# Kernel optimization log

Measured on AMD Instinct MI355X. Metric: run time of the kernel, lower is better.

## Reference

```python
import jax, jax.numpy as jnp
import numpy as np

HID_DIM = 1024
B, S = 8, 2048
SCALE = float(np.sqrt(HID_DIM))
NEG = -1e10


def setup_inputs() -> dict:
    key = jax.random.key(0)
    ks = jax.random.split(key, 13)
    d = HID_DIM
    std = 1.0 / np.sqrt(d)
    return {
        "query": jax.random.normal(ks[0], (B, S, d), jnp.float32),
        "key_": jax.random.normal(ks[1], (B, S, d), jnp.float32),
        "value": jax.random.normal(ks[2], (B, S, d), jnp.float32),
        "mask": jax.random.randint(ks[3], (B, S), 0, 2, jnp.int32),
        "Wq": jax.random.uniform(ks[4], (d, d), jnp.float32, -std, std),
        "bq": jax.random.uniform(ks[5], (d,), jnp.float32, -std, std),
        "Wk": jax.random.uniform(ks[6], (d, d), jnp.float32, -std, std),
        "bk": jax.random.uniform(ks[7], (d,), jnp.float32, -std, std),
        "Wv": jax.random.uniform(ks[8], (d, d), jnp.float32, -std, std),
        "bv": jax.random.uniform(ks[9], (d,), jnp.float32, -std, std),
        "Wfc": jax.random.uniform(ks[10], (d, d), jnp.float32, -std, std),
        "bfc": jax.random.uniform(ks[11], (d,), jnp.float32, -std, std),
    }


def reference(query, key_, value, mask, Wq, bq, Wk, bk, Wv, bv, Wfc, bfc):
    # Linear projections (torch Linear: x @ W.T + b)
    Q = jnp.einsum("bsd,ed->bse", query, Wq) + bq
    K = jnp.einsum("bsd,ed->bse", key_, Wk) + bk
    V = jnp.einsum("bsd,ed->bse", value, Wv) + bv
    # Scaled dot-product energy: [B, S, S]
    energy = jnp.einsum("bqd,bkd->bqk", Q, K) / SCALE
    # Faithful to source: mask broadcast over last dim masks QUERY rows
    energy = jnp.where(mask[:, :, None] == 0, NEG, energy)
    attention = jax.nn.softmax(energy, axis=-1)  # dropout=0 (eval)
    x = jnp.einsum("bqk,bkd->bqd", attention, V)
    out = jnp.einsum("bsd,ed->bse", x, Wfc) + bfc
    return out
```

## Files before the change

kernel.cpp:

```cpp
#include <hip/hip_runtime.h>
#include <hip/hip_bf16.h>


#define DEVINL __device__ __forceinline__

typedef __bf16 bf16x8 __attribute__((ext_vector_type(8)));
typedef float f32x4 __attribute__((ext_vector_type(4)));

static constexpr int Bb = 8;
static constexpr int S = 2048;
static constexpr int D = 1024;

DEVINL unsigned short f32_to_bf16(float f) {
  unsigned u = __float_as_uint(f);
  u = (u + 0x7FFFu + ((u >> 16) & 1u)) >> 16;
  return (unsigned short)u;
}
DEVINL float bflo(unsigned u) { return __uint_as_float(u << 16); }
DEVINL float bfhi(unsigned u) { return __uint_as_float(u & 0xFFFF0000u); }

DEVINL void gload16(const unsigned short* g, char* l) {
  __builtin_amdgcn_global_load_lds((__attribute__((address_space(1))) void*)g,
                                   (__attribute__((address_space(3))) void*)l,
                                   16, 0, 0);
}
DEVINL void gload16u(const unsigned short* g, unsigned short* l) {
  gload16(g, (char*)l);
}

#define BAR() __builtin_amdgcn_s_barrier()
#define LGK0() asm volatile("s_waitcnt lgkmcnt(0)" ::: "memory")

#define PH_OPEN() \
  BAR();          \
  LGK0();         \
  __builtin_amdgcn_s_setprio(1)
#define PH_CLOSE()               \
  __builtin_amdgcn_s_setprio(0); \
  BAR()

#define MFMA_QUAD(A_, B_, MO, NO)                                              \
  {                                                                            \
    _Pragma("unroll") for (int mi_ = 0; mi_ < 4; mi_++) {                      \
      _Pragma("unroll") for (int nj_ = 0; nj_ < 2; nj_++) {                    \
        acc[(MO) + mi_][(NO) + nj_] = __builtin_amdgcn_mfma_f32_16x16x32_bf16( \
            A_[mi_][0], B_[nj_][0], acc[(MO) + mi_][(NO) + nj_], 0, 0, 0);     \
        acc[(MO) + mi_][(NO) + nj_] = __builtin_amdgcn_mfma_f32_16x16x32_bf16( \
            A_[mi_][1], B_[nj_][1], acc[(MO) + mi_][(NO) + nj_], 0, 0, 0);     \
      }                                                                        \
    }                                                                          \
  }

__global__ __launch_bounds__(256) void conv_f32_bf16(const float* __restrict__ in,
                                                     unsigned short* __restrict__ out,
                                                     int n8) {
  int i = blockIdx.x * 256 + threadIdx.x;
  int stride = gridDim.x * 256;
  for (; i < n8; i += stride) {
    const float4* p = (const float4*)in + (size_t)i * 2;
    float4 a = p[0], b = p[1];
    uint4 o;
    o.x = (unsigned)f32_to_bf16(a.x) | ((unsigned)f32_to_bf16(a.y) << 16);
    o.y = (unsigned)f32_to_bf16(a.z) | ((unsigned)f32_to_bf16(a.w) << 16);
    o.z = (unsigned)f32_to_bf16(b.x) | ((unsigned)f32_to_bf16(b.y) << 16);
    o.w = (unsigned)f32_to_bf16(b.z) | ((unsigned)f32_to_bf16(b.w) << 16);
    ((uint4*)out)[i] = o;
  }
}

__global__ __launch_bounds__(256) void tconv(const float* __restrict__ in,
                                             unsigned short* __restrict__ out,
                                             int R, int C) {
  __shared__ unsigned short t[64][72];
  const int c0 = blockIdx.x * 64, r0 = blockIdx.y * 64, b = blockIdx.z;
  in += (size_t)b * R * C;
  out += (size_t)b * R * C;
  const int tr = threadIdx.x >> 4;
  const int tc = threadIdx.x & 15;
#pragma unroll
  for (int i = 0; i < 4; i++) {
    int row = tr + i * 16;
    float4 v = *(const float4*)(in + (size_t)(r0 + row) * C + c0 + tc * 4);
    t[tc * 4 + 0][row] = f32_to_bf16(v.x);
    t[tc * 4 + 1][row] = f32_to_bf16(v.y);
    t[tc * 4 + 2][row] = f32_to_bf16(v.z);
    t[tc * 4 + 3][row] = f32_to_bf16(v.w);
  }
  __syncthreads();
  const int c = threadIdx.x >> 2, rs = (threadIdx.x & 3) * 16;
  unsigned short tmp[16];
#pragma unroll
  for (int j = 0; j < 16; j++) tmp[j] = t[c][rs + j];
  *(uint4*)(out + (size_t)(c0 + c) * R + r0 + rs) = *(const uint4*)&tmp[0];
  *(uint4*)(out + (size_t)(c0 + c) * R + r0 + rs + 8) = *(const uint4*)&tmp[8];
}

__global__ __launch_bounds__(256) void cvec_kernel(const float* __restrict__ Wfc,
                                                   const float* __restrict__ bv,
                                                   const float* __restrict__ bfc,
                                                   float* __restrict__ cv) {
  const int f = blockIdx.x;
  const float* row = Wfc + (size_t)f * 1024;
  float s = 0.f;
  for (int e = threadIdx.x; e < 1024; e += 256) s += row[e] * bv[e];
#pragma unroll
  for (int off = 32; off >= 1; off >>= 1) s += __shfl_xor(s, off);
  __shared__ float red[4];
  const int wave = threadIdx.x >> 6, lane = threadIdx.x & 63;
  if (lane == 0) red[wave] = s;
  __syncthreads();
  if (threadIdx.x == 0) cv[f] = red[0] + red[1] + red[2] + red[3] + bfc[f];
}

__global__ __launch_bounds__(256) void gvec_kernel(const unsigned short* __restrict__ WkT,
                                                   const float* __restrict__ bq,
                                                   float* __restrict__ g32) {
  const int e = blockIdx.x;
  const unsigned short* row = WkT + (size_t)e * 1024;
  const int j0 = threadIdx.x * 4;
  uint2 v = *(const uint2*)(row + j0);
  float4 b4 = *(const float4*)(bq + j0);
  float s = bflo(v.x) * b4.x + bfhi(v.x) * b4.y + bflo(v.y) * b4.z + bfhi(v.y) * b4.w;
#pragma unroll
  for (int off = 32; off >= 1; off >>= 1) s += __shfl_xor(s, off);
  __shared__ float red[4];
  const int wave = threadIdx.x >> 6, lane = threadIdx.x & 63;
  if (lane == 0) red[wave] = s;
  __syncthreads();
  if (threadIdx.x == 0) g32[e] = (red[0] + red[1] + red[2] + red[3]) * (1.0f / 32.0f);
}

__global__ __launch_bounds__(256) void wvec_kernel(const unsigned short* __restrict__ xk,
                                                   const float* __restrict__ g32,
                                                   float* __restrict__ w32) {
  const int row = blockIdx.x * 4 + (threadIdx.x >> 6);
  const int lane = threadIdx.x & 63;
  const unsigned short* r = xk + (size_t)row * 1024;
  float s = 0.f;
#pragma unroll
  for (int c = 0; c < 2; c++) {
    const int e0 = c * 512 + lane * 8;
    uint4 v = *(const uint4*)(r + e0);
    unsigned u[4] = {v.x, v.y, v.z, v.w};
#pragma unroll
    for (int i = 0; i < 4; i++) {
      float2 gg = *(const float2*)(g32 + e0 + i * 2);
      s += bflo(u[i]) * gg.x + bfhi(u[i]) * gg.y;
    }
  }
#pragma unroll
  for (int off = 32; off >= 1; off >>= 1) s += __shfl_xor(s, off);
  if (lane == 0) w32[row] = s;
}

__global__ __launch_bounds__(256) void rowinv_kernel(const float* __restrict__ partialT,
                                                     float* __restrict__ rowinv) {
  const int r = blockIdx.x * 256 + threadIdx.x;
  float s = 0.f;
#pragma unroll
  for (int c = 0; c < 16; c++) s += partialT[(size_t)c * 16384 + r];
  rowinv[r] = 1.0f / s;
}

__global__ __launch_bounds__(256) void gemm128(const unsigned short* __restrict__ A,
                                               const unsigned short* __restrict__ Bt,
                                               unsigned short* __restrict__ C,
                                               int M, int N, int K,
                                               long long bsA, long long bsB, long long bsC) {
  const int tid = threadIdx.x;
  const int wave = tid >> 6;
  const int lane = tid & 63;
  const int wr = wave >> 1, wc = wave & 1;
  const int m0 = blockIdx.y * 128, n0 = blockIdx.x * 128;
  A += (size_t)blockIdx.z * bsA;
  Bt += (size_t)blockIdx.z * bsB;
  C += (size_t)blockIdx.z * bsC;

  __shared__ unsigned short lds[2][2][128 * 32];

  const int srow = wave * 16 + (lane >> 2);
  const int scol = (lane & 3) * 8;
  const unsigned short* gA = A + (size_t)(m0 + srow) * K + scol;
  const unsigned short* gB = Bt + (size_t)(n0 + srow) * K + scol;

  f32x4 acc[4][4];
#pragma unroll
  for (int i = 0; i < 4; i++)
#pragma unroll
    for (int j = 0; j < 4; j++) acc[i][j] = (f32x4){0.f, 0.f, 0.f, 0.f};

  const int nk = K >> 5;
  auto stage = [&](int buf, int kt) {
    const unsigned short* a0 = gA + (size_t)kt * 32;
    const unsigned short* b0 = gB + (size_t)kt * 32;
    unsigned short* la = &lds[buf][0][wave * 512];
    unsigned short* lb = &lds[buf][1][wave * 512];
    gload16u(a0, la);
    gload16u(a0 + (size_t)64 * K, la + 2048);
    gload16u(b0, lb);
    gload16u(b0 + (size_t)64 * K, lb + 2048);
  };

  stage(0, 0);
  asm volatile("s_waitcnt vmcnt(0)" ::: "memory");
  __syncthreads();

  const int fm = lane & 15;
  const int fk = (lane >> 4) * 8;

  int cur = 0;
  for (int t = 0; t < nk; ++t) {
    if (t + 1 < nk) stage(cur ^ 1, t + 1);
    bf16x8 af[4], bfr[4];
#pragma unroll
    for (int i = 0; i < 4; i++)
      af[i] = *(const bf16x8*)&lds[cur][0][(wr * 64 + i * 16 + fm) * 32 + fk];
#pragma unroll
    for (int j = 0; j < 4; j++)
      bfr[j] = *(const bf16x8*)&lds[cur][1][(wc * 64 + j * 16 + fm) * 32 + fk];
#pragma unroll
    for (int i = 0; i < 4; i++)
#pragma unroll
      for (int j = 0; j < 4; j++)
        acc[i][j] = __builtin_amdgcn_mfma_f32_16x16x32_bf16(af[i], bfr[j], acc[i][j], 0, 0, 0);
    asm volatile("s_waitcnt vmcnt(0)" ::: "memory");
    __syncthreads();
    cur ^= 1;
  }

  const int en = n0 + wc * 64 + fm;
  const int em = m0 + wr * 64 + ((lane >> 4) << 2);
#pragma unroll
  for (int j = 0; j < 4; j++)
#pragma unroll
    for (int i = 0; i < 4; i++)
#pragma unroll
      for (int r = 0; r < 4; r++)
        C[(size_t)(em + i * 16 + r) * N + en + j * 16] = f32_to_bf16(acc[i][j][r]);
}

template <int OUTMODE, bool HAS_BIAS>
__global__ __launch_bounds__(512, 2) void gemm256(
    const unsigned short* __restrict__ A, const unsigned short* __restrict__ Bt,
    const float* __restrict__ bias, const int* __restrict__ msk,
    float* __restrict__ partial, void* __restrict__ Cv,
    int M, int N, int K, int lda, int ldb,
    long long bsA, long long bsB, long long bsC, float scale) {
  extern __shared__ char smem[];
  const int tid = threadIdx.x;
  const int wave = tid >> 6, lane = tid & 63;
  const int wr = wave >> 2, wc = wave & 3;

  const int gx = gridDim.x, gy = gridDim.y;
  const int nwg = gx * gy * (int)gridDim.z;
  const int wg = blockIdx.x + gx * (blockIdx.y + gy * blockIdx.z);
  const int swz = (wg & 7) * (nwg >> 3) + (wg >> 3);
  const int bx = swz % gx;
  const int rem = swz / gx;
  const int by = rem % gy;
  const int bz = rem / gy;

  const int m0 = by * 256, n0 = bx * 256;
  A += (size_t)bz * bsA;
  Bt += (size_t)bz * bsB;

  const int rl = lane >> 3;
  const int gl = (lane & 7) ^ rl;
  const unsigned short* gA = A + (size_t)(m0 + wave * 8 + rl) * lda + gl * 8;
  const unsigned short* gB = Bt + (size_t)(n0 + wave * 8 + rl) * ldb + gl * 8;

  auto stageA = [&](int db, int t, int h) {
    const unsigned short* g = gA + (size_t)(h * 128) * lda + (size_t)t * 64;
    char* l = smem + db * 65536 + h * 16384 + wave * 1024;
    gload16(g, l);
    gload16(g + (size_t)64 * lda, l + 8192);
  };
  auto stageB = [&](int db, int t, int h) {
    const unsigned short* g = gB + (size_t)(h * 128) * ldb + (size_t)t * 64;
    char* l = smem + db * 65536 + 32768 + h * 16384 + wave * 1024;
    gload16(g, l);
    gload16(g + (size_t)64 * ldb, l + 8192);
  };

  const int fr = lane & 15;
  const int fg = lane >> 4;
  auto readA = [&](int db, int mi, int kc) -> bf16x8 {
    const int row = wr * 128 + mi * 16 + fr;
    const int g = (kc * 4 + fg) ^ (row & 7);
    return *(const bf16x8*)(smem + db * 65536 + row * 128 + g * 16);
  };
  auto readB = [&](int db, int nj, int kc) -> bf16x8 {
    const int row = wc * 64 + nj * 16 + fr;
    const int g = (kc * 4 + fg) ^ (row & 7);
    return *(const bf16x8*)(smem + db * 65536 + 32768 + row * 128 + g * 16);
  };

  f32x4 acc[8][4];
#pragma unroll
  for (int i = 0; i < 8; i++)
#pragma unroll
    for (int j = 0; j < 4; j++) acc[i][j] = (f32x4){0.f, 0.f, 0.f, 0.f};

  stageA(0, 0, 0);
  stageA(0, 0, 1);
  stageB(0, 0, 0);
  stageB(0, 0, 1);
  stageB(1, 1, 0);
  stageB(1, 1, 1);
  stageA(1, 1, 0);
  stageA(1, 1, 1);
  asm volatile("s_waitcnt vmcnt(8)" ::: "memory");
  BAR();

  const int nt = K >> 6;
  const int niter = nt >> 1;

  for (int j = 0; j < niter; ++j) {
    const int t0 = 2 * j, t1 = 2 * j + 1;
    const bool more = (j + 1 < niter);
    bf16x8 a[4][2], b0[2][2], b1[2][2];

#pragma unroll
    for (int mi = 0; mi < 4; mi++) { a[mi][0] = readA(0, mi, 0); a[mi][1] = readA(0, mi, 1); }
#pragma unroll
    for (int nj = 0; nj < 2; nj++) { b0[nj][0] = readB(0, nj, 0); b0[nj][1] = readB(0, nj, 1); }
    asm volatile("s_waitcnt lgkmcnt(8)" ::: "memory");
    PH_OPEN();
    MFMA_QUAD(a, b0, 0, 0);
    PH_CLOSE();

#pragma unroll
    for (int nj = 0; nj < 2; nj++) { b1[nj][0] = readB(0, nj + 2, 0); b1[nj][1] = readB(0, nj + 2, 1); }
    PH_OPEN();
    MFMA_QUAD(a, b1, 0, 2);
    PH_CLOSE();

#pragma unroll
    for (int mi = 0; mi < 4; mi++) { a[mi][0] = readA(0, mi + 4, 0); a[mi][1] = readA(0, mi + 4, 1); }
    if (more) stageB(0, t0 + 2, 0);
    PH_OPEN();
    MFMA_QUAD(a, b0, 4, 0);
    PH_CLOSE();

    if (more) {
      stageB(0, t0 + 2, 1);
      stageA(0, t0 + 2, 0);
      stageA(0, t0 + 2, 1);
    }
    BAR();
    __builtin_amdgcn_s_setprio(1);
    MFMA_QUAD(a, b1, 4, 2);
    __builtin_amdgcn_s_setprio(0);
    if (more)
      asm volatile("s_waitcnt vmcnt(8)" ::: "memory");
    else
      asm volatile("s_waitcnt vmcnt(0)" ::: "memory");
    BAR();

#pragma unroll
    for (int mi = 0; mi < 4; mi++) { a[mi][0] = readA(1, mi, 0); a[mi][1] = readA(1, mi, 1); }
#pragma unroll
    for (int nj = 0; nj < 2; nj++) { b0[nj][0] = readB(1, nj, 0); b0[nj][1] = readB(1, nj, 1); }
    asm volatile("s_waitcnt lgkmcnt(8)" ::: "memory");
    PH_OPEN();
    MFMA_QUAD(a, b0, 0, 0);
    PH_CLOSE();

#pragma unroll
    for (int nj = 0; nj < 2; nj++) { b1[nj][0] = readB(1, nj + 2, 0); b1[nj][1] = readB(1, nj + 2, 1); }
    PH_OPEN();
    MFMA_QUAD(a, b1, 0, 2);
    PH_CLOSE();

#pragma unroll
    for (int mi = 0; mi < 4; mi++) { a[mi][0] = readA(1, mi + 4, 0); a[mi][1] = readA(1, mi + 4, 1); }
    if (more) stageB(1, t1 + 2, 0);
    PH_OPEN();
    MFMA_QUAD(a, b0, 4, 0);
    PH_CLOSE();

    if (more) {
      stageB(1, t1 + 2, 1);
      stageA(1, t1 + 2, 0);
      stageA(1, t1 + 2, 1);
    }
    BAR();
    __builtin_amdgcn_s_setprio(1);
    MFMA_QUAD(a, b1, 4, 2);
    __builtin_amdgcn_s_setprio(0);
    if (more)
      asm volatile("s_waitcnt vmcnt(8)" ::: "memory");
    else
      asm volatile("s_waitcnt vmcnt(0)" ::: "memory");
    BAR();
  }

  const int row0base = m0 + wr * 128 + fg * 4;
  const int colbase = n0 + wc * 64 + fr;

  if (OUTMODE == 6) {
    float* C = (float*)Cv + (size_t)bz * bsC;
#pragma unroll
    for (int mi = 0; mi < 8; mi++) {
      const int j0 = row0base + mi * 16;
      const float4 ri = *(const float4*)&partial[bz * 2048 + j0];
#pragma unroll
      for (int nj = 0; nj < 4; nj++) {
        const int col = colbase + nj * 16;
        const float cvv = HAS_BIAS ? bias[col] : 0.0f;
        C[(size_t)(j0 + 0) * N + col] = fmaf(acc[mi][nj][0], ri.x, cvv);
        C[(size_t)(j0 + 1) * N + col] = fmaf(acc[mi][nj][1], ri.y, cvv);
        C[(size_t)(j0 + 2) * N + col] = fmaf(acc[mi][nj][2], ri.z, cvv);
        C[(size_t)(j0 + 3) * N + col] = fmaf(acc[mi][nj][3], ri.w, cvv);
      }
    }
  } else {
    const int lcol = wc * 64 + fr;
    const int lrow0 = wr * 128 + fg * 4;
    int mk[4];
    float psum[4] = {0.f, 0.f, 0.f, 0.f};
    if (OUTMODE == 3) {
#pragma unroll
      for (int nj = 0; nj < 4; nj++) mk[nj] = msk[bz * 2048 + colbase + nj * 16];
    }
#pragma unroll
    for (int mi = 0; mi < 8; mi++) {
      const int lrow = lrow0 + mi * 16;
      float4 w4 = make_float4(0.f, 0.f, 0.f, 0.f);
      if (OUTMODE == 3) w4 = *(const float4*)&bias[bz * 2048 + row0base + mi * 16];
#pragma unroll
      for (int nj = 0; nj < 4; nj++) {
        float v0, v1, v2, v3;
        if (OUTMODE == 3) {
          v0 = mk[nj] ? __expf(fmaf(acc[mi][nj][0], scale, w4.x)) : 1.0f;
          v1 = mk[nj] ? __expf(fmaf(acc[mi][nj][1], scale, w4.y)) : 1.0f;
          v2 = mk[nj] ? __expf(fmaf(acc[mi][nj][2], scale, w4.z)) : 1.0f;
          v3 = mk[nj] ? __expf(fmaf(acc[mi][nj][3], scale, w4.w)) : 1.0f;
          psum[nj] += (v0 + v1) + (v2 + v3);
        } else {
          v0 = acc[mi][nj][0];
          v1 = acc[mi][nj][1];
          v2 = acc[mi][nj][2];
          v3 = acc[mi][nj][3];
        }
        unsigned lo = (unsigned)f32_to_bf16(v0) | ((unsigned)f32_to_bf16(v1) << 16);
        unsigned hi = (unsigned)f32_to_bf16(v2) | ((unsigned)f32_to_bf16(v3) << 16);
        const int c = lcol + nj * 16;
        const int byte = c * 512 + ((((lrow >> 3) ^ (c & 7)) << 4) | ((lrow & 4) << 1));
        *(uint2*)(smem + byte) = make_uint2(lo, hi);
      }
    }
    if (OUTMODE == 3) {
#pragma unroll
      for (int nj = 0; nj < 4; nj++) {
        psum[nj] += __shfl_xor(psum[nj], 16);
        psum[nj] += __shfl_xor(psum[nj], 32);
      }
      if (fg == 0) {
#pragma unroll
        for (int nj = 0; nj < 4; nj++)
          partial[(size_t)(by * 2 + wr) * 16384 + bz * 2048 + colbase + nj * 16] = psum[nj];
      }
    }
    __syncthreads();
    unsigned short* C = (unsigned short*)Cv + (size_t)bz * bsC;
    const int qh = wave * 2 + (lane >> 5);
    const int kl = (lane & 31) * 8;
#pragma unroll
    for (int p = 0; p < 16; p++) {
      const int ql = qh + p * 16;
      const int byte = ql * 512 + ((((kl >> 3) ^ (ql & 7)) << 4));
      uint4 vv = *(const uint4*)(smem + byte);
      *(uint4*)(C + (size_t)(n0 + ql) * M + m0 + kl) = vv;
    }
  }
}

extern "C" void kernel_launch(void* const* d_in, const int* in_sizes, int n_in,
                              void* d_out, int out_size, void* d_ws, size_t ws_size,
                              hipStream_t stream) {
  const float* q = (const float*)d_in[0];
  const float* k_ = (const float*)d_in[1];
  const float* v = (const float*)d_in[2];
  const int* msk = (const int*)d_in[3];
  const float* Wq = (const float*)d_in[4];
  const float* bq = (const float*)d_in[5];
  const float* Wk = (const float*)d_in[6];
  const float* Wv = (const float*)d_in[8];
  const float* bv = (const float*)d_in[9];
  const float* Wfc = (const float*)d_in[10];
  const float* bfc = (const float*)d_in[11];

  char* ws = (char*)d_ws;
  const size_t MB = 1u << 20;
  unsigned short* WkT = (unsigned short*)(ws + 0 * MB);
  unsigned short* WfcB = (unsigned short*)(ws + 2 * MB);
  unsigned short* WqT = (unsigned short*)(ws + 4 * MB);
  unsigned short* WvT = (unsigned short*)(ws + 6 * MB);
  unsigned short* Mt = (unsigned short*)(ws + 8 * MB);
  unsigned short* W2 = (unsigned short*)(ws + 10 * MB);
  float* partialT = (float*)(ws + 12 * MB);
  float* rowinv = (float*)(ws + 13 * MB);
  float* cv = (float*)(ws + 13 * MB + 256 * 1024);
  float* g32 = (float*)(ws + 13 * MB + 512 * 1024);
  float* w32 = (float*)(ws + 13 * MB + 768 * 1024);
  unsigned short* Qc = (unsigned short*)(ws + 16 * MB);
  unsigned short* xkB = (unsigned short*)(ws + 48 * MB);
  unsigned short* vpT = (unsigned short*)(ws + 80 * MB);
  unsigned short* xqB = (unsigned short*)(ws + 112 * MB);
  unsigned short* vB = (unsigned short*)(ws + 144 * MB);
  unsigned short* E = (unsigned short*)(ws + 112 * MB);

  const int NBS = Bb * S * D;

  auto conv = [&](const float* in, unsigned short* out, int n) {
    int n8 = n / 8;
    int blocks = (n8 + 255) / 256;
    if (blocks > 2048) blocks = 2048;
    conv_f32_bf16<<<dim3(blocks), dim3(256), 0, stream>>>(in, out, n8);
  };

  tconv<<<dim3(16, 16, 1), dim3(256), 0, stream>>>(Wq, WqT, D, D);
  tconv<<<dim3(16, 16, 1), dim3(256), 0, stream>>>(Wk, WkT, D, D);
  conv(Wfc, WfcB, D * D);
  tconv<<<dim3(16, 16, 1), dim3(256), 0, stream>>>(Wv, WvT, D, D);
  gemm128<<<dim3(8, 8, 2), dim3(256), 0, stream>>>(
      WkT, WqT, Mt, D, D, D, (long long)D * D, (long long)D * D, (long long)D * D);
  cvec_kernel<<<dim3(1024), dim3(256), 0, stream>>>(Wfc, bv, bfc, cv);
  gvec_kernel<<<dim3(1024), dim3(256), 0, stream>>>(WkT, bq, g32);

  const float invscale = 1.0f / 32.0f;

  conv(q, xqB, NBS);
  gemm256<1, false><<<dim3(64, 4, 1), dim3(512), 131072, stream>>>(
      Mt, xqB, nullptr, nullptr, nullptr, Qc, D, Bb * S, D, D, D, 0, 0, 0, 1.0f);
  conv(k_, xkB, NBS);
  wvec_kernel<<<dim3(4096), dim3(256), 0, stream>>>(xkB, g32, w32);
  conv(v, vB, NBS);
  gemm256<1, false><<<dim3(4, 64, 1), dim3(512), 131072, stream>>>(
      vB, W2, nullptr, nullptr, nullptr, vpT, Bb * S, D, D, D, D, 0, 0, 0, 1.0f);
  gemm256<3, false><<<dim3(8, 8, 8), dim3(512), 131072, stream>>>(
      xkB, Qc, w32, msk, partialT, E, S, S, D, D, D,
      (long long)S * D, (long long)S * D, (long long)S * S, invscale);
  rowinv_kernel<<<dim3(64), dim3(256), 0, stream>>>(partialT, rowinv);
  gemm256<6, true><<<dim3(4, 8, 8), dim3(512), 131072, stream>>>(
      E, vpT, cv, nullptr, rowinv, d_out, S, D, S, S, Bb * S,
      (long long)S * S, (long long)S, (long long)S * D, 1.0f);
}
```

Measured before the change: 328.2 us.

## Compact unmasked query rows and skip masked-row attention work

Scans the mask per batch to build compacted indices of unmasked query rows. Only those rows are converted, projected and run through the QK and PV GEMMs, and tiles past the padded count exit early. Masked query rows get a uniform softmax, so their output is the column mean of projected V plus bias, written by a separate fill kernel. The code also adds a 128-wide QK GEMM with a triple buffer and reorders A-tile staging in gemm256. The cost is several extra small kernels and data-dependent grid exits, which makes runtime depend on mask density.

```diff
diff --git a/kernel.cpp b/kernel.cpp
--- a/kernel.cpp
+++ b/kernel.cpp
@@ -153,12 +153,104 @@
   if (lane == 0) w32[row] = s;
 }
 
+__global__ __launch_bounds__(256) void mask_scan(const int* __restrict__ msk,
+                                                 int* __restrict__ qidx,
+                                                 int* __restrict__ midx,
+                                                 int* __restrict__ cnts) {
+  __shared__ int offs[257];
+  const int b = blockIdx.x;
+  const int* mrow = msk + b * 2048;
+  const int base = threadIdx.x * 8;
+  int m[8], c = 0;
+#pragma unroll
+  for (int i = 0; i < 8; i++) {
+    m[i] = mrow[base + i];
+    c += m[i];
+  }
+  offs[threadIdx.x + 1] = c;
+  __syncthreads();
+  if (threadIdx.x == 0) {
+    offs[0] = 0;
+    for (int j = 1; j <= 256; j++) offs[j] += offs[j - 1];
+    int tot = offs[256];
+    cnts[b] = tot;
+    cnts[8 + b] = (tot + 127) & ~127;
+    cnts[16 + b] = (tot + 255) & ~255;
+    cnts[24 + b] = 2048 - tot;
+  }
+  __syncthreads();
+  int u = offs[threadIdx.x];
+#pragma unroll
+  for (int i = 0; i < 8; i++) {
+    int idx = base + i;
+    if (m[i])
+      qidx[b * 2048 + (u++)] = idx;
+    else
+      midx[b * 2048 + (idx - u)] = idx;
+  }
+}
+
+__global__ __launch_bounds__(128) void compact_q(const float* __restrict__ q,
+                                                 const int* __restrict__ qidx,
+                                                 const int* __restrict__ cnts,
+                                                 unsigned short* __restrict__ xqC) {
+  const int r = blockIdx.x;
+  const int b = r >> 11, i = r & 2047;
+  if (i >= cnts[16 + b]) return;
+  unsigned short* dst = xqC + ((size_t)b * 2048 + i) * 1024;
+  if (i < cnts[b]) {
+    const float* src = q + ((size_t)b * 2048 + qidx[b * 2048 + i]) * 1024 + threadIdx.x * 8;
+    float4 a = *(const float4*)src;
+    float4 c = *(const float4*)(src + 4);
+    uint4 o;
+    o.x = (unsigned)f32_to_bf16(a.x) | ((unsigned)f32_to_bf16(a.y) << 16);
+    o.y = (unsigned)f32_to_bf16(a.z) | ((unsigned)f32_to_bf16(a.w) << 16);
+    o.z = (unsigned)f32_to_bf16(c.x) | ((unsigned)f32_to_bf16(c.y) << 16);
+    o.w = (unsigned)f32_to_bf16(c.z) | ((unsigned)f32_to_bf16(c.w) << 16);
+    ((uint4*)dst)[threadIdx.x] = o;
+  } else {
+    ((uint4*)dst)[threadIdx.x] = make_uint4(0, 0, 0, 0);
+  }
+}
+
+__global__ __launch_bounds__(64) void colmean_kernel(const unsigned short* __restrict__ vpT,
+                                                     const float* __restrict__ cv,
+                                                     float* __restrict__ cm) {
+  const int f = blockIdx.x, b = blockIdx.y;
+  const unsigned short* base = vpT + (size_t)f * 16384 + b * 2048 + threadIdx.x * 32;
+  float s = 0.f;
+#pragma unroll
+  for (int c = 0; c < 4; c++) {
+    uint4 v = ((const uint4*)base)[c];
+    unsigned u[4] = {v.x, v.y, v.z, v.w};
+#pragma unroll
+    for (int i = 0; i < 4; i++) s += bflo(u[i]) + bfhi(u[i]);
+  }
+#pragma unroll
+  for (int off = 32; off >= 1; off >>= 1) s += __shfl_xor(s, off);
+  if (threadIdx.x == 0) cm[b * 1024 + f] = s * (1.0f / 2048.0f) + cv[f];
+}
+
+__global__ __launch_bounds__(128) void fill_masked(const int* __restrict__ midx,
+                                                   const int* __restrict__ cnts,
+                                                   const float* __restrict__ cm,
+                                                   float* __restrict__ out) {
+  const int r = blockIdx.x;
+  const int b = r >> 11, j = r & 2047;
+  if (j >= cnts[24 + b]) return;
+  const int qr = midx[b * 2048 + j];
+  float* dst = out + ((size_t)b * 2048 + qr) * 1024 + threadIdx.x * 8;
+  const float* src = cm + b * 1024 + threadIdx.x * 8;
+  *(float4*)dst = *(const float4*)src;
+  *(float4*)(dst + 4) = *(const float4*)(src + 4);
+}
+
 __global__ __launch_bounds__(256) void rowinv_kernel(const float* __restrict__ partialT,
                                                      float* __restrict__ rowinv) {
   const int r = blockIdx.x * 256 + threadIdx.x;
   float s = 0.f;
 #pragma unroll
-  for (int c = 0; c < 16; c++) s += partialT[(size_t)c * 16384 + r];
+  for (int c = 0; c < 32; c++) s += partialT[(size_t)c * 16384 + r];
   rowinv[r] = 1.0f / s;
 }
 
@@ -239,12 +331,150 @@
         C[(size_t)(em + i * 16 + r) * N + en + j * 16] = f32_to_bf16(acc[i][j][r]);
 }
 
-template <int OUTMODE, bool HAS_BIAS>
+__global__ __launch_bounds__(512, 1) void gemmE(
+    const unsigned short* __restrict__ A, const unsigned short* __restrict__ Bt,
+    const float* __restrict__ w32, const int* __restrict__ cnts,
+    float* __restrict__ partialT, unsigned short* __restrict__ E, float scale) {
+  extern __shared__ char smem[];
+  const int tid = threadIdx.x;
+  const int wave = tid >> 6, lane = tid & 63;
+  const int wrM = wave >> 1, wcN = wave & 1;
+
+  const int nwg = 16 * 8 * 8;
+  const int wg = blockIdx.x + 16 * (blockIdx.y + 8 * blockIdx.z);
+  const int swz = (wg & 7) * (nwg >> 3) + (wg >> 3);
+  const int bx = swz % 16;
+  const int rem = swz / 16;
+  const int by = rem % 8;
+  const int bz = rem / 8;
+
+  const int n0 = bx * 128;
+  if (n0 >= cnts[8 + bz]) return;
+  const int m0 = by * 256;
+  A += (size_t)bz * 2048 * 1024;
+  Bt += (size_t)bz * 2048 * 1024;
+
+  const int rl = lane >> 3;
+  const int gl = (lane & 7) ^ rl;
+  const unsigned short* gA = A + (size_t)(m0 + wave * 8 + rl) * 1024 + gl * 8;
+  const unsigned short* gB = Bt + (size_t)(n0 + wave * 8 + rl) * 1024 + gl * 8;
+
+  auto stage = [&](int db, int t) {
+    char* base = smem + db * 49152;
+    const unsigned short* ga = gA + (size_t)t * 64;
+    const unsigned short* gb = gB + (size_t)t * 64;
+#pragma unroll
+    for (int c = 0; c < 4; c++)
+      gload16(ga + (size_t)c * 64 * 1024, base + c * 8192 + wave * 1024);
+#pragma unroll
+    for (int c = 0; c < 2; c++)
+      gload16(gb + (size_t)c * 64 * 1024, base + 32768 + c * 8192 + wave * 1024);
+  };
+
+  const int fr = lane & 15;
+  const int fg = lane >> 4;
+  auto readA = [&](int db, int mi, int kc) -> bf16x8 {
+    const int row = wrM * 64 + mi * 16 + fr;
+    const int g = (kc * 4 + fg) ^ (row & 7);
+    return *(const bf16x8*)(smem + db * 49152 + row * 128 + g * 16);
+  };
+  auto readB = [&](int db, int nj, int kc) -> bf16x8 {
+    const int row = wcN * 64 + nj * 16 + fr;
+    const int g = (kc * 4 + fg) ^ (row & 7);
+    return *(const bf16x8*)(smem + db * 49152 + 32768 + row * 128 + g * 16);
+  };
+
+  f32x4 acc[4][4];
+#pragma unroll
+  for (int i = 0; i < 4; i++)
+#pragma unroll
+    for (int j = 0; j < 4; j++) acc[i][j] = (f32x4){0.f, 0.f, 0.f, 0.f};
+
+  const int nt = 16;
+  stage(0, 0);
+  stage(1, 1);
+  asm volatile("s_waitcnt vmcnt(6)" ::: "memory");
+  BAR();
+
+  for (int t = 0; t < nt; ++t) {
+    const int db = t % 3;
+    bf16x8 a[4][2], b0[2][2], b1[2][2];
+#pragma unroll
+    for (int mi = 0; mi < 4; mi++) { a[mi][0] = readA(db, mi, 0); a[mi][1] = readA(db, mi, 1); }
+#pragma unroll
+    for (int nj = 0; nj < 2; nj++) { b0[nj][0] = readB(db, nj, 0); b0[nj][1] = readB(db, nj, 1); }
+    BAR();
+    LGK0();
+    if (t + 2 < nt) stage((t + 2) % 3, t + 2);
+    __builtin_amdgcn_s_setprio(1);
+    MFMA_QUAD(a, b0, 0, 0);
+    __builtin_amdgcn_s_setprio(0);
+    BAR();
+#pragma unroll
+    for (int nj = 0; nj < 2; nj++) { b1[nj][0] = readB(db, nj + 2, 0); b1[nj][1] = readB(db, nj + 2, 1); }
+    BAR();
+    LGK0();
+    __builtin_amdgcn_s_setprio(1);
+    MFMA_QUAD(a, b1, 0, 2);
+    __builtin_amdgcn_s_setprio(0);
+    if (t + 2 < nt)
+      asm volatile("s_waitcnt vmcnt(6)" ::: "memory");
+    else
+      asm volatile("s_waitcnt vmcnt(0)" ::: "memory");
+    BAR();
+  }
+
+  const int keyrow0 = m0 + wrM * 64 + fg * 4;
+  const int colq = wcN * 64 + fr;
+  float psum[4] = {0.f, 0.f, 0.f, 0.f};
+#pragma unroll
+  for (int mi = 0; mi < 4; mi++) {
+    const int krow = keyrow0 + mi * 16;
+    const float4 w4 = *(const float4*)&w32[bz * 2048 + krow];
+    const int lrow = wrM * 64 + fg * 4 + mi * 16;
+#pragma unroll
+    for (int nj = 0; nj < 4; nj++) {
+      float p0 = __expf(fmaf(acc[mi][nj][0], scale, w4.x));
+      float p1 = __expf(fmaf(acc[mi][nj][1], scale, w4.y));
+      float p2 = __expf(fmaf(acc[mi][nj][2], scale, w4.z));
+      float p3 = __expf(fmaf(acc[mi][nj][3], scale, w4.w));
+      psum[nj] += (p0 + p1) + (p2 + p3);
+      unsigned lo = (unsigned)f32_to_bf16(p0) | ((unsigned)f32_to_bf16(p1) << 16);
+      unsigned hi = (unsigned)f32_to_bf16(p2) | ((unsigned)f32_to_bf16(p3) << 16);
+      const int c = colq + nj * 16;
+      const int byte = c * 512 + ((((lrow >> 3) ^ (c & 7)) << 4) | ((lrow & 4) << 1));
+      *(uint2*)(smem + byte) = make_uint2(lo, hi);
+    }
+  }
+#pragma unroll
+  for (int nj = 0; nj < 4; nj++) {
+    psum[nj] += __shfl_xor(psum[nj], 16);
+    psum[nj] += __shfl_xor(psum[nj], 32);
+  }
+  if (fg == 0) {
+#pragma unroll
+    for (int nj = 0; nj < 4; nj++)
+      partialT[(size_t)(by * 4 + wrM) * 16384 + bz * 2048 + n0 + colq + nj * 16] = psum[nj];
+  }
+  __syncthreads();
+  unsigned short* Eb = E + (size_t)bz * S * S;
+  const int qh = wave * 2 + (lane >> 5);
+  const int kl = (lane & 31) * 8;
+#pragma unroll
+  for (int p = 0; p < 8; p++) {
+    const int ql = qh + p * 16;
+    const int byte = ql * 512 + ((((kl >> 3) ^ (ql & 7)) << 4));
+    uint4 vv = *(const uint4*)(smem + byte);
+    *(uint4*)(Eb + (size_t)(n0 + ql) * 2048 + m0 + kl) = vv;
+  }
+}
+
+template <int OUTMODE, bool HAS_BIAS, int EXITMODE>
 __global__ __launch_bounds__(512, 2) void gemm256(
     const unsigned short* __restrict__ A, const unsigned short* __restrict__ Bt,
-    const float* __restrict__ bias, const int* __restrict__ msk,
-    float* __restrict__ partial, void* __restrict__ Cv,
-    int M, int N, int K, int lda, int ldb,
+    const float* __restrict__ bias, const int* __restrict__ cnts,
+    const int* __restrict__ qidx, float* __restrict__ partial,
+    void* __restrict__ Cv, int M, int N, int K, int lda, int ldb,
     long long bsA, long long bsB, long long bsC, float scale) {
   extern __shared__ char smem[];
   const int tid = threadIdx.x;
@@ -261,6 +491,11 @@
   const int bz = rem / gy;
 
   const int m0 = by * 256, n0 = bx * 256;
+  if (EXITMODE == 1) {
+    if ((n0 & 2047) >= cnts[16 + (n0 >> 11)]) return;
+  } else if (EXITMODE == 2) {
+    if (m0 >= cnts[16 + bz]) return;
+  }
   A += (size_t)bz * bsA;
   Bt += (size_t)bz * bsB;
 
@@ -307,9 +542,7 @@
   stageB(0, 0, 1);
   stageB(1, 1, 0);
   stageB(1, 1, 1);
-  stageA(1, 1, 0);
-  stageA(1, 1, 1);
-  asm volatile("s_waitcnt vmcnt(8)" ::: "memory");
+  asm volatile("s_waitcnt vmcnt(4)" ::: "memory");
   BAR();
 
   const int nt = K >> 6;
@@ -324,6 +557,7 @@
     for (int mi = 0; mi < 4; mi++) { a[mi][0] = readA(0, mi, 0); a[mi][1] = readA(0, mi, 1); }
 #pragma unroll
     for (int nj = 0; nj < 2; nj++) { b0[nj][0] = readB(0, nj, 0); b0[nj][1] = readB(0, nj, 1); }
+    stageA(1, t1, 0);
     asm volatile("s_waitcnt lgkmcnt(8)" ::: "memory");
     PH_OPEN();
     MFMA_QUAD(a, b0, 0, 0);
@@ -331,6 +565,7 @@
 
 #pragma unroll
     for (int nj = 0; nj < 2; nj++) { b1[nj][0] = readB(0, nj + 2, 0); b1[nj][1] = readB(0, nj + 2, 1); }
+    stageA(1, t1, 1);
     PH_OPEN();
     MFMA_QUAD(a, b1, 0, 2);
     PH_CLOSE();
@@ -342,17 +577,13 @@
     MFMA_QUAD(a, b0, 4, 0);
     PH_CLOSE();
 
-    if (more) {
-      stageB(0, t0 + 2, 1);
-      stageA(0, t0 + 2, 0);
-      stageA(0, t0 + 2, 1);
-    }
+    if (more) stageB(0, t0 + 2, 1);
     BAR();
     __builtin_amdgcn_s_setprio(1);
     MFMA_QUAD(a, b1, 4, 2);
     __builtin_amdgcn_s_setprio(0);
     if (more)
-      asm volatile("s_waitcnt vmcnt(8)" ::: "memory");
+      asm volatile("s_waitcnt vmcnt(4)" ::: "memory");
     else
       asm volatile("s_waitcnt vmcnt(0)" ::: "memory");
     BAR();
@@ -361,6 +592,7 @@
     for (int mi = 0; mi < 4; mi++) { a[mi][0] = readA(1, mi, 0); a[mi][1] = readA(1, mi, 1); }
 #pragma unroll
     for (int nj = 0; nj < 2; nj++) { b0[nj][0] = readB(1, nj, 0); b0[nj][1] = readB(1, nj, 1); }
+    if (more) stageA(0, t0 + 2, 0);
     asm volatile("s_waitcnt lgkmcnt(8)" ::: "memory");
     PH_OPEN();
     MFMA_QUAD(a, b0, 0, 0);
@@ -368,6 +600,7 @@
 
 #pragma unroll
     for (int nj = 0; nj < 2; nj++) { b1[nj][0] = readB(1, nj + 2, 0); b1[nj][1] = readB(1, nj + 2, 1); }
+    if (more) stageA(0, t0 + 2, 1);
     PH_OPEN();
     MFMA_QUAD(a, b1, 0, 2);
     PH_CLOSE();
@@ -379,19 +612,12 @@
     MFMA_QUAD(a, b0, 4, 0);
     PH_CLOSE();
 
-    if (more) {
-      stageB(1, t1 + 2, 1);
-      stageA(1, t1 + 2, 0);
-      stageA(1, t1 + 2, 1);
-    }
+    if (more) stageB(1, t1 + 2, 1);
     BAR();
     __builtin_amdgcn_s_setprio(1);
     MFMA_QUAD(a, b1, 4, 2);
     __builtin_amdgcn_s_setprio(0);
-    if (more)
-      asm volatile("s_waitcnt vmcnt(8)" ::: "memory");
-    else
-      asm volatile("s_waitcnt vmcnt(0)" ::: "memory");
+    asm volatile("s_waitcnt vmcnt(4)" ::: "memory");
     BAR();
   }
 
@@ -400,66 +626,48 @@
 
   if (OUTMODE == 6) {
     float* C = (float*)Cv + (size_t)bz * bsC;
+    const int* qx = qidx + bz * 2048;
+    const int cb = cnts[bz];
 #pragma unroll
     for (int mi = 0; mi < 8; mi++) {
       const int j0 = row0base + mi * 16;
       const float4 ri = *(const float4*)&partial[bz * 2048 + j0];
+      int qr[4];
+      bool ok[4];
+#pragma unroll
+      for (int r = 0; r < 4; r++) {
+        ok[r] = (j0 + r) < cb;
+        qr[r] = ok[r] ? qx[j0 + r] : 0;
+      }
 #pragma unroll
       for (int nj = 0; nj < 4; nj++) {
         const int col = colbase + nj * 16;
         const float cvv = HAS_BIAS ? bias[col] : 0.0f;
-        C[(size_t)(j0 + 0) * N + col] = fmaf(acc[mi][nj][0], ri.x, cvv);
-        C[(size_t)(j0 + 1) * N + col] = fmaf(acc[mi][nj][1], ri.y, cvv);
-        C[(size_t)(j0 + 2) * N + col] = fmaf(acc[mi][nj][2], ri.z, cvv);
-        C[(size_t)(j0 + 3) * N + col] = fmaf(acc[mi][nj][3], ri.w, cvv);
+        if (ok[0]) C[(size_t)qr[0] * N + col] = fmaf(acc[mi][nj][0], ri.x, cvv);
+        if (ok[1]) C[(size_t)qr[1] * N + col] = fmaf(acc[mi][nj][1], ri.y, cvv);
+        if (ok[2]) C[(size_t)qr[2] * N + col] = fmaf(acc[mi][nj][2], ri.z, cvv);
+        if (ok[3]) C[(size_t)qr[3] * N + col] = fmaf(acc[mi][nj][3], ri.w, cvv);
       }
     }
   } else {
     const int lcol = wc * 64 + fr;
     const int lrow0 = wr * 128 + fg * 4;
-    int mk[4];
-    float psum[4] = {0.f, 0.f, 0.f, 0.f};
-    if (OUTMODE == 3) {
-#pragma unroll
-      for (int nj = 0; nj < 4; nj++) mk[nj] = msk[bz * 2048 + colbase + nj * 16];
-    }
 #pragma unroll
     for (int mi = 0; mi < 8; mi++) {
       const int lrow = lrow0 + mi * 16;
-      float4 w4 = make_float4(0.f, 0.f, 0.f, 0.f);
-      if (OUTMODE == 3) w4 = *(const float4*)&bias[bz * 2048 + row0base + mi * 16];
+      float4 bw = make_float4(0.f, 0.f, 0.f, 0.f);
+      if (HAS_BIAS) bw = *(const float4*)&bias[row0base + mi * 16];
 #pragma unroll
       for (int nj = 0; nj < 4; nj++) {
-        float v0, v1, v2, v3;
-        if (OUTMODE == 3) {
-          v0 = mk[nj] ? __expf(fmaf(acc[mi][nj][0], scale, w4.x)) : 1.0f;
-          v1 = mk[nj] ? __expf(fmaf(acc[mi][nj][1], scale, w4.y)) : 1.0f;
-          v2 = mk[nj] ? __expf(fmaf(acc[mi][nj][2], scale, w4.z)) : 1.0f;
-          v3 = mk[nj] ? __expf(fmaf(acc[mi][nj][3], scale, w4.w)) : 1.0f;
-          psum[nj] += (v0 + v1) + (v2 + v3);
-        } else {
-          v0 = acc[mi][nj][0];
-          v1 = acc[mi][nj][1];
-          v2 = acc[mi][nj][2];
-          v3 = acc[mi][nj][3];
-        }
+        float v0 = acc[mi][nj][0] + bw.x;
+        float v1 = acc[mi][nj][1] + bw.y;
+        float v2 = acc[mi][nj][2] + bw.z;
+        float v3 = acc[mi][nj][3] + bw.w;
         unsigned lo = (unsigned)f32_to_bf16(v0) | ((unsigned)f32_to_bf16(v1) << 16);
         unsigned hi = (unsigned)f32_to_bf16(v2) | ((unsigned)f32_to_bf16(v3) << 16);
         const int c = lcol + nj * 16;
         const int byte = c * 512 + ((((lrow >> 3) ^ (c & 7)) << 4) | ((lrow & 4) << 1));
         *(uint2*)(smem + byte) = make_uint2(lo, hi);
-      }
-    }
-    if (OUTMODE == 3) {
-#pragma unroll
-      for (int nj = 0; nj < 4; nj++) {
-        psum[nj] += __shfl_xor(psum[nj], 16);
-        psum[nj] += __shfl_xor(psum[nj], 32);
-      }
-      if (fg == 0) {
-#pragma unroll
-        for (int nj = 0; nj < 4; nj++)
-          partial[(size_t)(by * 2 + wr) * 16384 + bz * 2048 + colbase + nj * 16] = psum[nj];
       }
     }
     __syncthreads();
@@ -493,6 +701,7 @@
 
   char* ws = (char*)d_ws;
   const size_t MB = 1u << 20;
+  const size_t KB = 1u << 10;
   unsigned short* WkT = (unsigned short*)(ws + 0 * MB);
   unsigned short* WfcB = (unsigned short*)(ws + 2 * MB);
   unsigned short* WqT = (unsigned short*)(ws + 4 * MB);
@@ -500,14 +709,18 @@
   unsigned short* Mt = (unsigned short*)(ws + 8 * MB);
   unsigned short* W2 = (unsigned short*)(ws + 10 * MB);
   float* partialT = (float*)(ws + 12 * MB);
-  float* rowinv = (float*)(ws + 13 * MB);
-  float* cv = (float*)(ws + 13 * MB + 256 * 1024);
-  float* g32 = (float*)(ws + 13 * MB + 512 * 1024);
-  float* w32 = (float*)(ws + 13 * MB + 768 * 1024);
+  float* rowinv = (float*)(ws + 14 * MB);
+  float* cv = (float*)(ws + 14 * MB + 64 * KB);
+  float* g32 = (float*)(ws + 14 * MB + 128 * KB);
+  float* w32 = (float*)(ws + 14 * MB + 192 * KB);
+  int* qidx = (int*)(ws + 14 * MB + 256 * KB);
+  int* midx = (int*)(ws + 14 * MB + 320 * KB);
+  int* cnts = (int*)(ws + 14 * MB + 384 * KB);
+  float* cm = (float*)(ws + 14 * MB + 512 * KB);
   unsigned short* Qc = (unsigned short*)(ws + 16 * MB);
   unsigned short* xkB = (unsigned short*)(ws + 48 * MB);
   unsigned short* vpT = (unsigned short*)(ws + 80 * MB);
-  unsigned short* xqB = (unsigned short*)(ws + 112 * MB);
+  unsigned short* xqC = (unsigned short*)(ws + 112 * MB);
   unsigned short* vB = (unsigned short*)(ws + 144 * MB);
   unsigned short* E = (unsigned short*)(ws + 112 * MB);
 
@@ -529,21 +742,26 @@
   cvec_kernel<<<dim3(1024), dim3(256), 0, stream>>>(Wfc, bv, bfc, cv);
   gvec_kernel<<<dim3(1024), dim3(256), 0, stream>>>(WkT, bq, g32);
 
+  mask_scan<<<dim3(8), dim3(256), 0, stream>>>(msk, qidx, midx, cnts);
+  compact_q<<<dim3(16384), dim3(128), 0, stream>>>(q, qidx, cnts, xqC);
+
   const float invscale = 1.0f / 32.0f;
 
-  conv(q, xqB, NBS);
-  gemm256<1, false><<<dim3(64, 4, 1), dim3(512), 131072, stream>>>(
-      Mt, xqB, nullptr, nullptr, nullptr, Qc, D, Bb * S, D, D, D, 0, 0, 0, 1.0f);
+  gemm256<1, false, 1><<<dim3(64, 4, 1), dim3(512), 131072, stream>>>(
+      Mt, xqC, nullptr, cnts, nullptr, nullptr, Qc, D, Bb * S, D, D, D,
+      0, 0, 0, 1.0f);
   conv(k_, xkB, NBS);
   wvec_kernel<<<dim3(4096), dim3(256), 0, stream>>>(xkB, g32, w32);
   conv(v, vB, NBS);
-  gemm256<1, false><<<dim3(4, 64, 1), dim3(512), 131072, stream>>>(
-      vB, W2, nullptr, nullptr, nullptr, vpT, Bb * S, D, D, D, D, 0, 0, 0, 1.0f);
-  gemm256<3, false><<<dim3(8, 8, 8), dim3(512), 131072, stream>>>(
-      xkB, Qc, w32, msk, partialT, E, S, S, D, D, D,
-      (long long)S * D, (long long)S * D, (long long)S * S, invscale);
+  gemm256<1, false, 0><<<dim3(4, 64, 1), dim3(512), 131072, stream>>>(
+      vB, W2, nullptr, nullptr, nullptr, nullptr, vpT, Bb * S, D, D, D, D,
+      0, 0, 0, 1.0f);
+  colmean_kernel<<<dim3(1024, 8), dim3(64), 0, stream>>>(vpT, cv, cm);
+  gemmE<<<dim3(16, 8, 8), dim3(512), 147456, stream>>>(
+      xkB, Qc, w32, cnts, partialT, E, invscale);
   rowinv_kernel<<<dim3(64), dim3(256), 0, stream>>>(partialT, rowinv);
-  gemm256<6, true><<<dim3(4, 8, 8), dim3(512), 131072, stream>>>(
-      E, vpT, cv, nullptr, rowinv, d_out, S, D, S, S, Bb * S,
+  gemm256<6, true, 2><<<dim3(4, 8, 8), dim3(512), 131072, stream>>>(
+      E, vpT, cv, cnts, qidx, rowinv, d_out, S, D, S, S, Bb * S,
       (long long)S * S, (long long)S, (long long)S * D, 1.0f);
-}
+  fill_masked<<<dim3(16384), dim3(128), 0, stream>>>(midx, cnts, cm, (float*)d_out);
+}
```

After: 319.4 us. 2.7% less time.
